# Kernel tuning notes

Measured on AMD Instinct MI355X. Metric: run time of the kernel, lower is better.

## Reference

```python
import jax, jax.numpy as jnp
import numpy as np

B, S, F = 4, 2048, 1024

def setup_inputs() -> dict:
    key = jax.random.key(0)
    ks = jax.random.split(key, 9)
    s = 1.0 / np.sqrt(F)
    return {
        "q": jax.random.normal(ks[0], (B, S, F), jnp.float32),
        "k": jax.random.normal(ks[1], (B, S, F), jnp.float32),
        "v": jax.random.normal(ks[2], (B, S, F), jnp.float32),
        "Wq": jax.random.normal(ks[3], (F, F), jnp.float32) * s,
        "bq": jax.random.normal(ks[4], (F,), jnp.float32) * s,
        "Wk": jax.random.normal(ks[5], (F, F), jnp.float32) * s,
        "bk": jax.random.normal(ks[6], (F,), jnp.float32) * s,
        "Wv": jax.random.normal(ks[7], (F, F), jnp.float32) * s,
        "bv": jax.random.normal(ks[8], (F,), jnp.float32) * s,
    }

def reference(q, k, v, Wq, bq, Wk, bk, Wv, bv):
    # Linear layers: x @ W^T + b (torch nn.Linear convention)
    qp = jnp.einsum('bsf,gf->bsg', q, Wq) + bq
    kp = jnp.einsum('bsf,gf->bsg', k, Wk) + bk
    vp = jnp.einsum('bsf,gf->bsg', v, Wv) + bv
    # Unscaled attention (no 1/sqrt(d)), as in the original module
    attn = jax.nn.softmax(jnp.einsum('bqf,bkf->bqk', qp, kp), axis=-1)
    return jnp.einsum('bqk,bkf->bqf', attn, vp) + q
```

## Files before the change

kernel.cpp:

```cpp
#include <hip/hip_runtime.h>

typedef unsigned short u16;
typedef __bf16 bf16x8 __attribute__((ext_vector_type(8)));
typedef float f32x4 __attribute__((ext_vector_type(4)));
typedef u16 u16x8 __attribute__((ext_vector_type(8)));

union B8 { u16x8 u; bf16x8 b; };

__device__ __forceinline__ u16 f2b(float f){
  unsigned u = __float_as_uint(f);
  return (u16)((u + 0x7FFFu + ((u >> 16) & 1u)) >> 16);
}
__device__ __forceinline__ float b2f(u16 h){ return __uint_as_float(((unsigned)h) << 16); }

__device__ __forceinline__ void gload16(const u16* g, u16* l){
  __builtin_amdgcn_global_load_lds((const __attribute__((address_space(1))) void*)g,
                                   (__attribute__((address_space(3))) void*)l, 16, 0, 0);
}

__global__ __launch_bounds__(256) void split_all_kernel(
    const float* __restrict__ q, const float* __restrict__ k, const float* __restrict__ v,
    const float* __restrict__ Wq, const float* __restrict__ Wk, const float* __restrict__ Wv,
    u16* __restrict__ q_pair, u16* __restrict__ k_pair, u16* __restrict__ v_b,
    u16* __restrict__ Wq_pair, u16* __restrict__ Wk_pair, u16* __restrict__ Wv_b)
{
  int b = blockIdx.x;
  const float* src; u16* dst; bool dual; long base;
  if      (b < 4096)  { src = q;  dst = q_pair;  dual = true;  base = b; }
  else if (b < 8192)  { src = k;  dst = k_pair;  dual = true;  base = b - 4096; }
  else if (b < 12288) { src = v;  dst = v_b;     dual = false; base = b - 8192; }
  else if (b < 12800) { src = Wq; dst = Wq_pair; dual = true;  base = b - 12288; }
  else if (b < 13312) { src = Wk; dst = Wk_pair; dual = true;  base = b - 12800; }
  else                { src = Wv; dst = Wv_b;    dual = false; base = b - 13312; }
  long i = base * 256 + threadIdx.x;
  float4 x0 = ((const float4*)src)[2 * i];
  float4 x1 = ((const float4*)src)[2 * i + 1];
  float xs[8] = {x0.x, x0.y, x0.z, x0.w, x1.x, x1.y, x1.z, x1.w};
  u16x8 h, l;
  #pragma unroll
  for (int j = 0; j < 8; j++){ h[j] = f2b(xs[j]); l[j] = f2b(xs[j] - b2f(h[j])); }
  if (dual){
    ((u16x8*)dst)[2 * i]     = h;
    ((u16x8*)dst)[2 * i + 1] = l;
  } else {
    ((u16x8*)dst)[i] = h;
  }
}

__device__ __forceinline__ void xcd_remap(int& tx, int& ty, int& tz){
  const int GX = gridDim.x, GY = gridDim.y;
  int b  = blockIdx.x + GX * (blockIdx.y + GY * blockIdx.z);
  int NB = GX * GY * gridDim.z;
  int rank = (b & 7) * (NB >> 3) + (b >> 3);
  int pz = GX * GY;
  tz = rank / pz;
  int r = rank - tz * pz;
  ty = r / GX;
  tx = r - ty * GX;
}

constexpr int BM = 128, BN = 128, BK = 32;

__device__ __forceinline__ int lds1_idx(int row, int g){
  return row * 32 + g * 8;
}
__device__ __forceinline__ int lds2_idx(int row, int g){
  return row * 64 + (((g ^ (row & 7)) & 7) << 3);
}

template<bool DUAL, int EPI>
__global__ __launch_bounds__(256, 4)
void gemm_nt(const u16* __restrict__ A, const u16* __restrict__ Bm,
             const float* __restrict__ bias, const float* __restrict__ biasB,
             const float* __restrict__ residual,
             void* __restrict__ out0,
             int M, int N, int K,
             long sAb, long sBb, long sOb, long sRb, int seq)
{
  constexpr int RW = DUAL ? 64 : 32;
  __shared__ u16 lds[2][BM * RW];

  int tx, ty, tz; xcd_remap(tx, ty, tz);
  const int t = threadIdx.x;
  const int tileM = ty * BM;
  const int tileN = tx * BN;
  const long rs = DUAL ? 2L * K : (long)K;

  const u16* gA = A  + tz * sAb + (long)tileM * rs;
  const u16* gB = Bm + tz * sBb + (long)tileN * rs;

  const int wave = t >> 6, lane = t & 63;
  const int wm = (wave >> 1) * 64, wn = (wave & 1) * 64;
  const int lr = lane & 15;
  const int lg = lane >> 4;

  const u16 *pa, *pb;
  long jstride;
  int  ldsbase, ldsstep, nissue, kadv;
  if (DUAL){
    const int lr8 = lane >> 3, sl = lane & 7;
    const int g = sl ^ lr8;
    pa = gA + (long)(wave * 32 + lr8) * rs + g * 8;
    pb = gB + (long)(wave * 32 + lr8) * rs + g * 8;
    jstride = 8 * rs;
    ldsbase = (wave * 32) * 64; ldsstep = 8 * 64;
    nissue = 4; kadv = 64;
  } else {
    pa = gA + (long)(wave * 32 + (lane >> 2)) * rs + (lane & 3) * 8;
    pb = gB + (long)(wave * 32 + (lane >> 2)) * rs + (lane & 3) * 8;
    jstride = 16 * rs;
    ldsbase = (wave * 32) * 32; ldsstep = 16 * 32;
    nissue = 2; kadv = 32;
  }

  f32x4 acc[4][4] = {};

  for (int k0 = 0; k0 < K; k0 += BK){
    __syncthreads();
    #pragma unroll 4
    for (int j = 0; j < nissue; j++){
      gload16(pa + j * jstride, &lds[0][ldsbase + j * ldsstep]);
      gload16(pb + j * jstride, &lds[1][ldsbase + j * ldsstep]);
    }
    pa += kadv; pb += kadv;
    __syncthreads();

    if (DUAL){
      B8 ah[4], al[4], bh[4], bl[4];
      #pragma unroll
      for (int mt = 0; mt < 4; mt++){
        int row = wm + mt * 16 + lr;
        ah[mt].u = *(const u16x8*)&lds[0][lds2_idx(row, lg * 2)];
        al[mt].u = *(const u16x8*)&lds[0][lds2_idx(row, lg * 2 + 1)];
      }
      #pragma unroll
      for (int nt = 0; nt < 4; nt++){
        int row = wn + nt * 16 + lr;
        bh[nt].u = *(const u16x8*)&lds[1][lds2_idx(row, lg * 2)];
        bl[nt].u = *(const u16x8*)&lds[1][lds2_idx(row, lg * 2 + 1)];
      }
      #pragma unroll
      for (int mt = 0; mt < 4; mt++){
        #pragma unroll
        for (int nt = 0; nt < 4; nt++){
          acc[mt][nt] = __builtin_amdgcn_mfma_f32_16x16x32_bf16(ah[mt].b, bh[nt].b, acc[mt][nt], 0, 0, 0);
          acc[mt][nt] = __builtin_amdgcn_mfma_f32_16x16x32_bf16(ah[mt].b, bl[nt].b, acc[mt][nt], 0, 0, 0);
          acc[mt][nt] = __builtin_amdgcn_mfma_f32_16x16x32_bf16(al[mt].b, bh[nt].b, acc[mt][nt], 0, 0, 0);
        }
      }
    } else {
      B8 af[4], bf[4];
      #pragma unroll
      for (int mt = 0; mt < 4; mt++)
        af[mt].u = *(const u16x8*)&lds[0][lds1_idx(wm + mt * 16 + lr, lg)];
      #pragma unroll
      for (int nt = 0; nt < 4; nt++)
        bf[nt].u = *(const u16x8*)&lds[1][lds1_idx(wn + nt * 16 + lr, lg)];
      #pragma unroll
      for (int mt = 0; mt < 4; mt++)
        #pragma unroll
        for (int nt = 0; nt < 4; nt++)
          acc[mt][nt] = __builtin_amdgcn_mfma_f32_16x16x32_bf16(af[mt].b, bf[nt].b, acc[mt][nt], 0, 0, 0);
    }
  }

  const int rq = lg * 4;
  const float* bp = (tz && biasB) ? biasB : bias;
  #pragma unroll
  for (int nt = 0; nt < 4; nt++){
    const int n = tileN + wn + nt * 16 + lr;
    const float bv = (EPI <= 1) ? bp[n] : 0.f;
    #pragma unroll
    for (int mt = 0; mt < 4; mt++){
      #pragma unroll
      for (int r = 0; r < 4; r++){
        const int m = tileM + wm + mt * 16 + rq + r;
        float val = acc[mt][nt][r] + bv;
        if (EPI == 0){
          u16 h = f2b(val);
          u16* o = (u16*)out0 + (long)tz * sOb + (long)m * 2 * N + ((n >> 3) << 4) + (n & 7);
          o[0] = h;
          o[8] = f2b(val - b2f(h));
        } else if (EPI == 1){
          long idx = (long)(m / seq) * ((long)N * seq) + (long)n * seq + (m % seq);
          ((u16*)out0)[idx] = f2b(val);
        } else if (EPI == 2){
          ((float*)out0)[(long)tz * sOb + (long)m * N + n] = val;
        } else {
          float res = residual[(long)tz * sRb + (long)m * N + n];
          ((float*)out0)[(long)tz * sOb + (long)m * N + n] = val + res;
        }
      }
    }
  }
}

__global__ __launch_bounds__(256)
void softmax_kernel(const float* __restrict__ S, u16* __restrict__ P, int n){
  const long row = blockIdx.x;
  const float* r = S + row * (long)n;
  const int t = threadIdx.x;
  float v[8];
  float mx = -3.0e38f;
  #pragma unroll
  for (int i = 0; i < 8; i++){ v[i] = r[t + (i << 8)]; mx = fmaxf(mx, v[i]); }
  #pragma unroll
  for (int off = 32; off > 0; off >>= 1) mx = fmaxf(mx, __shfl_xor(mx, off, 64));
  __shared__ float red[8];
  const int wave = t >> 6;
  if ((t & 63) == 0) red[wave] = mx;
  __syncthreads();
  mx = fmaxf(fmaxf(red[0], red[1]), fmaxf(red[2], red[3]));
  float s = 0.f;
  #pragma unroll
  for (int i = 0; i < 8; i++){ v[i] = __expf(v[i] - mx); s += v[i]; }
  #pragma unroll
  for (int off = 32; off > 0; off >>= 1) s += __shfl_xor(s, off, 64);
  if ((t & 63) == 0) red[4 + wave] = s;
  __syncthreads();
  s = red[4] + red[5] + red[6] + red[7];
  const float inv = 1.f / s;
  u16* pr = P + row * (long)n;
  #pragma unroll
  for (int i = 0; i < 8; i++) pr[t + (i << 8)] = f2b(v[i] * inv);
}

extern "C" void kernel_launch(void* const* d_in, const int* in_sizes, int n_in,
                              void* d_out, int out_size, void* d_ws, size_t ws_size,
                              hipStream_t stream){
  (void)in_sizes; (void)n_in; (void)out_size; (void)ws_size;
  const float* q  = (const float*)d_in[0];
  const float* k  = (const float*)d_in[1];
  const float* v  = (const float*)d_in[2];
  const float* Wq = (const float*)d_in[3];
  const float* bq = (const float*)d_in[4];
  const float* Wk = (const float*)d_in[5];
  const float* bk = (const float*)d_in[6];
  const float* Wv = (const float*)d_in[7];
  const float* bv = (const float*)d_in[8];
  float* out = (float*)d_out;

  const int B = 4, S = 2048, F = 1024;
  const long NSF = (long)B * S * F;
  const long NFF = (long)F * F;
  const long NSS = (long)B * S * S;

  char* w = (char*)d_ws;
  auto alloc = [&](long bytes) -> char* {
    char* p = w; w += (bytes + 255) & ~(long)255; return p;
  };
  u16* qp_pair = (u16*)alloc(4 * NSF * 2);
  u16* kp_pair = qp_pair + 2 * NSF;
  u16* vpT     = (u16*)alloc(NSF * 2);
  char* zone2 = alloc(NSS * 2 + NSS * 4);
  u16*   attn   = (u16*)zone2;
  float* scores = (float*)(zone2 + NSS * 2);
  u16* q_pair  = (u16*)zone2;
  u16* k_pair  = q_pair + 2 * NSF;
  u16* v_b     = k_pair + 2 * NSF;
  u16* Wq_pair = v_b + NSF;
  u16* Wk_pair = Wq_pair + 2 * NFF;
  u16* Wv_b    = Wk_pair + 2 * NFF;

  dim3 blk(256);

  split_all_kernel<<<dim3(13824), blk, 0, stream>>>(
      q, k, v, Wq, Wk, Wv, q_pair, k_pair, v_b, Wq_pair, Wk_pair, Wv_b);

  gemm_nt<true, 0><<<dim3(F / BN, (B * S) / BM, 2), blk, 0, stream>>>(
      q_pair, Wq_pair, bq, bk, nullptr, qp_pair,
      B * S, F, F, 2 * NSF, 2 * NFF, 2 * NSF, 0, S);

  gemm_nt<false, 1><<<dim3(F / BN, (B * S) / BM, 1), blk, 0, stream>>>(
      v_b, Wv_b, bv, nullptr, nullptr, vpT,
      B * S, F, F, 0, 0, 0, 0, S);

  gemm_nt<true, 2><<<dim3(S / BN, S / BM, B), blk, 0, stream>>>(
      qp_pair, kp_pair, nullptr, nullptr, nullptr, scores,
      S, S, F, (long)S * 2 * F, (long)S * 2 * F, (long)S * S, 0, S);

  softmax_kernel<<<dim3(B * S), blk, 0, stream>>>(scores, attn, S);

  gemm_nt<false, 3><<<dim3(F / BN, S / BM, B), blk, 0, stream>>>(
      attn, vpT, nullptr, nullptr, q, out,
      S, F, S, (long)S * S, (long)F * S, (long)S * F, (long)S * F, S);
}
```

Measured before the change: 454.3 us.

## Fold Q/K projections into a single WqᵀWk matrix with key-side bias

Reassociates the score computation so q is multiplied by a precomputed 1024x1024 matrix WqᵀWk instead of projecting both q and k separately. Bias terms are reduced to a per-key vector k·(Wkᵀbq) added in the scores epilogue, and terms constant across a softmax row are dropped. This removes one full-size projection GEMM at the cost of a small split-K GEMM, a reduction kernel, a transposing weight prep and a serial bias dot-product kernel. Numerical error changes because the fused matrix is itself rounded to a bf16 hi/lo pair.

After: 463.2 us. No clear change (+2.0%).

```diff
diff --git a/kernel.cpp b/kernel.cpp
--- a/kernel.cpp
+++ b/kernel.cpp
@@ -18,33 +18,118 @@
                                    (__attribute__((address_space(3))) void*)l, 16, 0, 0);
 }
 
-__global__ __launch_bounds__(256) void split_all_kernel(
-    const float* __restrict__ q, const float* __restrict__ k, const float* __restrict__ v,
-    const float* __restrict__ Wq, const float* __restrict__ Wk, const float* __restrict__ Wv,
-    u16* __restrict__ q_pair, u16* __restrict__ k_pair, u16* __restrict__ v_b,
-    u16* __restrict__ Wq_pair, u16* __restrict__ Wk_pair, u16* __restrict__ Wv_b)
+__global__ __launch_bounds__(256) void prep_kernel(
+    const float* __restrict__ v, const float* __restrict__ Wv,
+    const float* __restrict__ Wq, const float* __restrict__ Wk,
+    const float* __restrict__ bq,
+    u16* __restrict__ v_b, u16* __restrict__ Wv_b,
+    u16* __restrict__ WqT_pair, u16* __restrict__ WkT_pair, float* __restrict__ b)
 {
-  int b = blockIdx.x;
-  const float* src; u16* dst; bool dual; long base;
-  if      (b < 4096)  { src = q;  dst = q_pair;  dual = true;  base = b; }
-  else if (b < 8192)  { src = k;  dst = k_pair;  dual = true;  base = b - 4096; }
-  else if (b < 12288) { src = v;  dst = v_b;     dual = false; base = b - 8192; }
-  else if (b < 12800) { src = Wq; dst = Wq_pair; dual = true;  base = b - 12288; }
-  else if (b < 13312) { src = Wk; dst = Wk_pair; dual = true;  base = b - 12800; }
-  else                { src = Wv; dst = Wv_b;    dual = false; base = b - 13312; }
-  long i = base * 256 + threadIdx.x;
+  __shared__ float lds[64][65];
+  const int blk = blockIdx.x, t = threadIdx.x;
+  if (blk < 4608){
+    const float* src; u16* dst; long base;
+    if (blk < 4096){ src = v;  dst = v_b;  base = blk; }
+    else           { src = Wv; dst = Wv_b; base = blk - 4096; }
+    long i = base * 256 + t;
+    float4 x0 = ((const float4*)src)[2 * i];
+    float4 x1 = ((const float4*)src)[2 * i + 1];
+    float xs[8] = {x0.x, x0.y, x0.z, x0.w, x1.x, x1.y, x1.z, x1.w};
+    u16x8 h;
+    #pragma unroll
+    for (int j = 0; j < 8; j++) h[j] = f2b(xs[j]);
+    ((u16x8*)dst)[i] = h;
+  } else if (blk < 5120){
+    int tt = blk - 4608;
+    const float* W = (tt >> 8) ? Wk : Wq;
+    u16* outp      = (tt >> 8) ? WkT_pair : WqT_pair;
+    int t16 = tt & 255, g0 = (t16 >> 4) * 64, f0 = (t16 & 15) * 64;
+    int c4 = (t & 15) * 4, r0 = t >> 4;
+    #pragma unroll
+    for (int it = 0; it < 4; it++){
+      int r = r0 + it * 16;
+      float4 x = *(const float4*)&W[(long)(g0 + r) * 1024 + f0 + c4];
+      lds[r][c4] = x.x; lds[r][c4+1] = x.y; lds[r][c4+2] = x.z; lds[r][c4+3] = x.w;
+    }
+    __syncthreads();
+    #pragma unroll
+    for (int it = 0; it < 2; it++){
+      int task = t + it * 256;
+      int fl = task >> 3, gi = task & 7;
+      u16x8 h, l;
+      #pragma unroll
+      for (int jj = 0; jj < 8; jj++){
+        float xv = lds[gi * 8 + jj][fl];
+        h[jj] = f2b(xv); l[jj] = f2b(xv - b2f(h[jj]));
+      }
+      u16* o = outp + (long)(f0 + fl) * 2048 + ((g0 >> 3) + gi) * 16;
+      *(u16x8*)o = h;
+      *(u16x8*)(o + 8) = l;
+    }
+  } else {
+    int e = (blk - 5120) * 256 + t;
+    float acc = 0.f;
+    for (int g = 0; g < 1024; g++) acc += Wk[(long)g * 1024 + e] * bq[g];
+    b[e] = acc;
+  }
+}
+
+__global__ __launch_bounds__(256) void split_qk_kernel(
+    const float* __restrict__ q, const float* __restrict__ kk,
+    const float* __restrict__ b,
+    u16* __restrict__ q_pair, u16* __restrict__ k_pair, float* __restrict__ kb)
+{
+  const int blk = blockIdx.x, t = threadIdx.x;
+  const bool isK = blk >= 4096;
+  const float* src = isK ? kk : q;
+  u16* dst = isK ? k_pair : q_pair;
+  long base = isK ? blk - 4096 : blk;
+  long i = base * 256 + t;
   float4 x0 = ((const float4*)src)[2 * i];
   float4 x1 = ((const float4*)src)[2 * i + 1];
   float xs[8] = {x0.x, x0.y, x0.z, x0.w, x1.x, x1.y, x1.z, x1.w};
   u16x8 h, l;
   #pragma unroll
   for (int j = 0; j < 8; j++){ h[j] = f2b(xs[j]); l[j] = f2b(xs[j] - b2f(h[j])); }
-  if (dual){
-    ((u16x8*)dst)[2 * i]     = h;
-    ((u16x8*)dst)[2 * i + 1] = l;
-  } else {
-    ((u16x8*)dst)[i] = h;
-  }
+  ((u16x8*)dst)[2 * i]     = h;
+  ((u16x8*)dst)[2 * i + 1] = l;
+  if (isK){
+    const int f = (t & 127) * 8;
+    float d = 0.f;
+    #pragma unroll
+    for (int j = 0; j < 8; j++) d += xs[j] * b[f + j];
+    #pragma unroll
+    for (int off = 32; off > 0; off >>= 1) d += __shfl_xor(d, off, 64);
+    __shared__ float red[4];
+    if ((t & 63) == 0) red[t >> 6] = d;
+    __syncthreads();
+    if (t == 0)   kb[base * 2]     = red[0] + red[1];
+    if (t == 128) kb[base * 2 + 1] = red[2] + red[3];
+  }
+}
+
+__global__ __launch_bounds__(256) void reduce_split_kernel(
+    const float* __restrict__ part, u16* __restrict__ out_pair, long nper)
+{
+  long i = (long)blockIdx.x * 256 + threadIdx.x;
+  float s[8];
+  #pragma unroll
+  for (int j = 0; j < 8; j++) s[j] = 0.f;
+  #pragma unroll
+  for (int z = 0; z < 4; z++){
+    float4 a0 = ((const float4*)(part + z * nper))[2 * i];
+    float4 a1 = ((const float4*)(part + z * nper))[2 * i + 1];
+    s[0]+=a0.x; s[1]+=a0.y; s[2]+=a0.z; s[3]+=a0.w;
+    s[4]+=a1.x; s[5]+=a1.y; s[6]+=a1.z; s[7]+=a1.w;
+  }
+  u16x8 h, l;
+  #pragma unroll
+  for (int j = 0; j < 8; j++){ h[j] = f2b(s[j]); l[j] = f2b(s[j] - b2f(h[j])); }
+  long e = (i * 8) >> 10;
+  long g = i & 127;
+  u16* o = out_pair + e * 2048 + g * 16;
+  *(u16x8*)o = h;
+  *(u16x8*)(o + 8) = l;
 }
 
 __device__ __forceinline__ void xcd_remap(int& tx, int& ty, int& tz){
@@ -61,9 +146,7 @@
 
 constexpr int BM = 128, BN = 128, BK = 32;
 
-__device__ __forceinline__ int lds1_idx(int row, int g){
-  return row * 32 + g * 8;
-}
+__device__ __forceinline__ int lds1_idx(int row, int g){ return row * 32 + g * 8; }
 __device__ __forceinline__ int lds2_idx(int row, int g){
   return row * 64 + (((g ^ (row & 7)) & 7) << 3);
 }
@@ -71,10 +154,9 @@
 template<bool DUAL, int EPI>
 __global__ __launch_bounds__(256, 4)
 void gemm_nt(const u16* __restrict__ A, const u16* __restrict__ Bm,
-             const float* __restrict__ bias, const float* __restrict__ biasB,
-             const float* __restrict__ residual,
+             const float* __restrict__ bias, const float* __restrict__ residual,
              void* __restrict__ out0,
-             int M, int N, int K,
+             int M, int N, int K, int Krow,
              long sAb, long sBb, long sOb, long sRb, int seq)
 {
   constexpr int RW = DUAL ? 64 : 32;
@@ -84,7 +166,7 @@
   const int t = threadIdx.x;
   const int tileM = ty * BM;
   const int tileN = tx * BN;
-  const long rs = DUAL ? 2L * K : (long)K;
+  const long rs = DUAL ? 2L * Krow : (long)Krow;
 
   const u16* gA = A  + tz * sAb + (long)tileM * rs;
   const u16* gB = Bm + tz * sBb + (long)tileN * rs;
@@ -165,11 +247,12 @@
   }
 
   const int rq = lg * 4;
-  const float* bp = (tz && biasB) ? biasB : bias;
   #pragma unroll
   for (int nt = 0; nt < 4; nt++){
     const int n = tileN + wn + nt * 16 + lr;
-    const float bv = (EPI <= 1) ? bp[n] : 0.f;
+    float bv = 0.f;
+    if (EPI <= 1 && bias) bv = bias[n];
+    if (EPI == 2 && bias) bv = bias[(long)tz * N + n];
     #pragma unroll
     for (int mt = 0; mt < 4; mt++){
       #pragma unroll
@@ -235,7 +318,6 @@
   const float* Wq = (const float*)d_in[3];
   const float* bq = (const float*)d_in[4];
   const float* Wk = (const float*)d_in[5];
-  const float* bk = (const float*)d_in[6];
   const float* Wv = (const float*)d_in[7];
   const float* bv = (const float*)d_in[8];
   float* out = (float*)d_out;
@@ -249,39 +331,51 @@
   auto alloc = [&](long bytes) -> char* {
     char* p = w; w += (bytes + 255) & ~(long)255; return p;
   };
-  u16* qp_pair = (u16*)alloc(4 * NSF * 2);
-  u16* kp_pair = qp_pair + 2 * NSF;
-  u16* vpT     = (u16*)alloc(NSF * 2);
+  u16*   tmp_pair = (u16*)alloc(2 * NSF * 2);
+  u16*   k_pair   = (u16*)alloc(2 * NSF * 2);
+  u16*   vpT      = (u16*)alloc(NSF * 2);
+  float* kb       = (float*)alloc((long)B * S * 4);
   char* zone2 = alloc(NSS * 2 + NSS * 4);
   u16*   attn   = (u16*)zone2;
   float* scores = (float*)(zone2 + NSS * 2);
-  u16* q_pair  = (u16*)zone2;
-  u16* k_pair  = q_pair + 2 * NSF;
-  u16* v_b     = k_pair + 2 * NSF;
-  u16* Wq_pair = v_b + NSF;
-  u16* Wk_pair = Wq_pair + 2 * NFF;
-  u16* Wv_b    = Wk_pair + 2 * NFF;
+  u16*   q_pair   = (u16*)zone2;
+  char*  z3       = zone2 + NSS * 2;
+  u16*   v_b      = (u16*)z3;
+  u16*   Wv_b     = (u16*)(z3 + NSF * 2);
+  u16*   WqT_pair = (u16*)(z3 + NSF * 2 + NFF * 2);
+  u16*   WkT_pair = WqT_pair + 2 * NFF;
+  float* b_vec    = (float*)(WkT_pair + 2 * NFF);
+  float* Mt_part  = (float*)((char*)b_vec + 4096);
+  u16*   Mt_pair  = (u16*)((char*)Mt_part + 4 * NFF * 4);
 
   dim3 blk(256);
 
-  split_all_kernel<<<dim3(13824), blk, 0, stream>>>(
-      q, k, v, Wq, Wk, Wv, q_pair, k_pair, v_b, Wq_pair, Wk_pair, Wv_b);
-
-  gemm_nt<true, 0><<<dim3(F / BN, (B * S) / BM, 2), blk, 0, stream>>>(
-      q_pair, Wq_pair, bq, bk, nullptr, qp_pair,
-      B * S, F, F, 2 * NSF, 2 * NFF, 2 * NSF, 0, S);
+  prep_kernel<<<dim3(5124), blk, 0, stream>>>(
+      v, Wv, Wq, Wk, bq, v_b, Wv_b, WqT_pair, WkT_pair, b_vec);
+
+  split_qk_kernel<<<dim3(8192), blk, 0, stream>>>(q, k, b_vec, q_pair, k_pair, kb);
+
+  gemm_nt<true, 2><<<dim3(F / BN, F / BM, 4), blk, 0, stream>>>(
+      WkT_pair, WqT_pair, nullptr, nullptr, Mt_part,
+      F, F, 256, F, 512, 512, NFF, 0, S);
+
+  reduce_split_kernel<<<dim3(512), blk, 0, stream>>>(Mt_part, Mt_pair, NFF);
+
+  gemm_nt<true, 0><<<dim3(F / BN, (B * S) / BM, 1), blk, 0, stream>>>(
+      q_pair, Mt_pair, nullptr, nullptr, tmp_pair,
+      B * S, F, F, F, 0, 0, 0, 0, S);
 
   gemm_nt<false, 1><<<dim3(F / BN, (B * S) / BM, 1), blk, 0, stream>>>(
-      v_b, Wv_b, bv, nullptr, nullptr, vpT,
-      B * S, F, F, 0, 0, 0, 0, S);
+      v_b, Wv_b, bv, nullptr, vpT,
+      B * S, F, F, F, 0, 0, 0, 0, S);
 
   gemm_nt<true, 2><<<dim3(S / BN, S / BM, B), blk, 0, stream>>>(
-      qp_pair, kp_pair, nullptr, nullptr, nullptr, scores,
-      S, S, F, (long)S * 2 * F, (long)S * 2 * F, (long)S * S, 0, S);
+      tmp_pair, k_pair, kb, nullptr, scores,
+      S, S, F, F, (long)S * 2 * F, (long)S * 2 * F, (long)S * S, 0, S);
 
   softmax_kernel<<<dim3(B * S), blk, 0, stream>>>(scores, attn, S);
 
   gemm_nt<false, 3><<<dim3(F / BN, S / BM, B), blk, 0, stream>>>(
-      attn, vpT, nullptr, nullptr, q, out,
-      S, F, S, (long)S * S, (long)F * S, (long)S * F, (long)S * F, S);
-}
+      attn, vpT, nullptr, q, out,
+      S, F, S, S, (long)S * S, (long)F * S, (long)S * F, (long)S * F, S);
+}
```
